# Kernel optimization log

Hardware: AMD Instinct MI355X
Metric: run time of the kernel (lower is better)

Reference implementation:

```python
import jax, jax.numpy as jnp
import numpy as np
from jax import lax

T, B, K, H, L = 256, 64, 1024, 1024, 3

def setup_inputs() -> dict:
    key = jax.random.key(0)
    ks = jax.random.split(key, 6)
    x = jax.random.normal(ks[0], (T, B, K), dtype=jnp.float32)
    h0 = jax.random.normal(ks[1], (L, B, H), dtype=jnp.float32) * 0.1
    # xavier-ish / orthogonal-ish scale for stability
    w_ih = jax.random.normal(ks[2], (L, 3 * H, K), dtype=jnp.float32) * (1.0 / np.sqrt(K))
    w_hh = jax.random.normal(ks[3], (L, 3 * H, H), dtype=jnp.float32) * (1.0 / np.sqrt(H))
    b_ih = jnp.zeros((L, 3 * H), dtype=jnp.float32)
    b_hh = jnp.zeros((L, 3 * H), dtype=jnp.float32)
    return {"x": x, "h0": h0, "w_ih": w_ih, "w_hh": w_hh, "b_ih": b_ih, "b_hh": b_hh}

def _gru_layer(x_seq, h_init, wih, whh, bih, bhh):
    # x_seq: [T,B,Kin], h_init: [B,H], wih: [3H,Kin], whh: [3H,H]
    Hd = h_init.shape[-1]
    # precompute input-to-hidden projections for all timesteps in one GEMM
    gi = jnp.einsum('tbk,gk->tbg', x_seq, wih) + bih  # [T,B,3H]

    def step(h, gi_t):
        gh = h @ whh.T + bhh  # [B,3H]
        r = jax.nn.sigmoid(gi_t[:, :Hd] + gh[:, :Hd])
        z = jax.nn.sigmoid(gi_t[:, Hd:2 * Hd] + gh[:, Hd:2 * Hd])
        n = jnp.tanh(gi_t[:, 2 * Hd:] + r * gh[:, 2 * Hd:])
        h_new = (1.0 - z) * n + z * h
        return h_new, h_new

    h_last, outs = lax.scan(step, h_init, gi)
    return h_last, outs  # [B,H], [T,B,H]

def reference(x, h0, w_ih, w_hh, b_ih, b_hh):
    layer_in = x
    h_n = []
    for l in range(w_ih.shape[0]):
        h_last, layer_in = _gru_layer(layer_in, h0[l], w_ih[l], w_hh[l], b_ih[l], b_hh[l])
        h_n.append(h_last)
    return jnp.stack(h_n, axis=0)  # [L,B,H]
```

## Files before the change

### kernel.cpp

```cpp
#include <hip/hip_runtime.h>
#include <hip/hip_bf16.h>

typedef __attribute__((ext_vector_type(8))) short bf16x8;
typedef __attribute__((ext_vector_type(4))) float f32x4;

#define T_STEPS 256
#define BATCH   64
#define KDIM    1024
#define HDIM    1024
#define NGATE   3072
#define LAYERS  3
#define SLOTE   (BATCH * HDIM)
#define RING_SLOTS (T_STEPS + 1)
#define WSZ     (192L * 32 * 64 * 8)
#define FSTRIDE 4

#define LDS_BS_BYTES  65536
#define LDS_WIS_BYTES 65536
#define LDS_GI_BYTES  (2 * 3 * 64 * 16 * 4)
#define LDS_TOTAL (LDS_BS_BYTES + LDS_WIS_BYTES + LDS_GI_BYTES)

#define MFMA16(a, b, c) __builtin_amdgcn_mfma_f32_16x16x32_bf16(a, b, c, 0, 0, 0)

__device__ __forceinline__ unsigned short f2b(float f) {
  union { float f; unsigned int u; } a; a.f = f;
  unsigned int u = a.u;
  unsigned int r = (u + 0x7FFFu + ((u >> 16) & 1u)) >> 16;
  return (unsigned short)r;
}
__device__ __forceinline__ void gload16(const void* gptr, void* ldsptr) {
  __builtin_amdgcn_global_load_lds(
      (const __attribute__((address_space(1))) unsigned int*)gptr,
      (__attribute__((address_space(3))) unsigned int*)ldsptr,
      16, 0, 0);
}

__global__ void f2b_kernel(const float* __restrict__ src,
                           unsigned short* __restrict__ dst, int n4) {
  int i = blockIdx.x * blockDim.x + threadIdx.x;
  if (i < n4) {
    float4 v = ((const float4*)src)[i];
    ushort4 o;
    o.x = f2b(v.x); o.y = f2b(v.y); o.z = f2b(v.z); o.w = f2b(v.w);
    ((ushort4*)dst)[i] = o;
  }
}

__global__ void swizzle_w(const float* __restrict__ w,
                          unsigned short* __restrict__ out) {
  long gid = (long)blockIdx.x * 256 + threadIdx.x;
  int lane = (int)(gid & 63);
  long rest = gid >> 6;
  int kc = (int)(rest & 31); rest >>= 5;
  int ntile = (int)(rest % 192); int l = (int)(rest / 192);
  int n  = ntile * 16 + (lane & 15);
  int k0 = kc * 32 + (lane >> 4) * 8;
  const float* src = w + (((long)l * NGATE + n) * KDIM + k0);
  unsigned short o[8];
#pragma unroll
  for (int j = 0; j < 8; j++) o[j] = f2b(src[j]);
  bf16x8 v = *(bf16x8*)o;
  *(bf16x8*)(out + gid * 8) = v;
}

__global__ __launch_bounds__(512, 2) void gru_fused(
    const unsigned short* __restrict__ xb,
    const unsigned short* __restrict__ wswhh,
    const unsigned short* __restrict__ wswih,
    const float* __restrict__ bih,
    const float* __restrict__ bhh,
    const float* __restrict__ h0,
    unsigned short* __restrict__ rings,
    float* __restrict__ hout,
    unsigned int* __restrict__ flags)
{
  extern __shared__ __align__(16) char smem[];
  unsigned short* Bs  = (unsigned short*)smem;
  unsigned short* Wis = (unsigned short*)(smem + LDS_BS_BYTES);
  float* gi_lds = (float*)(smem + LDS_BS_BYTES + LDS_WIS_BYTES);

  int l = blockIdx.x >> 6, g = blockIdx.x & 63;
  int tid = threadIdx.x, wave = tid >> 6, lane = tid & 63;
  int lg = lane >> 4;
  int rg = wave & 3;
  bool is_h = (wave < 4);
  int row = rg * 16 + (lane & 15);
  int cb  = g * 16 + lg * 4;

  const unsigned short* whh_l = wswhh + (size_t)l * WSZ;
  const unsigned short* wih_l = wswih + (size_t)l * WSZ;
  unsigned short* ring_l = rings + (size_t)l * RING_SLOTS * SLOTE;
  const unsigned short* prev_ring = rings + (size_t)(l - 1) * RING_SLOTS * SLOTE;
  unsigned int* fl = flags + (size_t)l * 64 * FSTRIDE;
  const unsigned int* fp = flags + (size_t)(l > 0 ? (l - 1) : 0) * 64 * FSTRIDE;

#pragma unroll
  for (int i = 0; i < 16; i++) {
    int p = wave * 16 + i;
    int gate = (p >> 5) & 1;
    int kc = p & 31;
    const unsigned short* src = (p < 64)
        ? whh_l + ((((long)gate * 64 + g) * 32 + kc) * 64 + lane) * 8
        : wih_l + ((((long)gate * 64 + g) * 32 + kc) * 64 + lane) * 8;
    unsigned short* dst = (p < 64)
        ? &Bs[(size_t)p * 512 + (size_t)lane * 8]
        : &Wis[(size_t)(p - 64) * 512 + (size_t)lane * 8];
    gload16(src, dst);
  }

  bf16x8 wn[32];
  {
    const unsigned short* base = is_h ? whh_l : wih_l;
#pragma unroll
    for (int kc = 0; kc < 32; kc++)
      wn[kc] = *(const bf16x8*)(base + ((((long)(2 * 64 + g)) * 32 + kc) * 64 + lane) * 8);
  }

  float br_[4], bz_[4], bi_n[4], bh_n[4];
  float h[4] = {0.f, 0.f, 0.f, 0.f};
  if (is_h) {
    const float* bh_l = bhh + l * NGATE;
    const float* bi_l = bih + l * NGATE;
    float4 bhr4 = *(const float4*)(bh_l + 0 * HDIM + cb);
    float4 bhz4 = *(const float4*)(bh_l + 1 * HDIM + cb);
    float4 bhn4 = *(const float4*)(bh_l + 2 * HDIM + cb);
    float4 bir4 = *(const float4*)(bi_l + 0 * HDIM + cb);
    float4 biz4 = *(const float4*)(bi_l + 1 * HDIM + cb);
    float4 bin4 = *(const float4*)(bi_l + 2 * HDIM + cb);
    br_[0] = bir4.x + bhr4.x; br_[1] = bir4.y + bhr4.y; br_[2] = bir4.z + bhr4.z; br_[3] = bir4.w + bhr4.w;
    bz_[0] = biz4.x + bhz4.x; bz_[1] = biz4.y + bhz4.y; bz_[2] = biz4.z + bhz4.z; bz_[3] = biz4.w + bhz4.w;
    bi_n[0] = bin4.x; bi_n[1] = bin4.y; bi_n[2] = bin4.z; bi_n[3] = bin4.w;
    bh_n[0] = bhn4.x; bh_n[1] = bhn4.y; bh_n[2] = bhn4.z; bh_n[3] = bhn4.w;

    float4 h4 = *(const float4*)(h0 + (size_t)l * SLOTE + (size_t)row * HDIM + cb);
    h[0] = h4.x; h[1] = h4.y; h[2] = h4.z; h[3] = h4.w;
    union { unsigned short us[4]; unsigned long long u; } pk;
#pragma unroll
    for (int r = 0; r < 4; r++) pk.us[r] = f2b(h[r]);
    unsigned short* slotT = ring_l + (size_t)T_STEPS * SLOTE;
    __hip_atomic_store((unsigned long long*)(slotT + (size_t)g * 1024 + (size_t)row * 16 + lg * 4),
                       pk.u, __ATOMIC_RELAXED, __HIP_MEMORY_SCOPE_AGENT);
  }

  f32x4 air, aiz, ain;
  auto xgemv = [&](int tt) {
    f32x4 z = {};
    air = z; aiz = z; ain = z;
    if (l == 0) {
      const unsigned short* xa_b = xb + (size_t)tt * SLOTE + (size_t)row * KDIM + lg * 8;
#pragma unroll
      for (int kb = 0; kb < 4; kb++) {
        bf16x8 xa[8];
#pragma unroll
        for (int j = 0; j < 8; j++)
          xa[j] = *(const bf16x8*)(xa_b + (size_t)(kb * 8 + j) * 32);
#pragma unroll
        for (int j = 0; j < 8; j++) {
          int kc = kb * 8 + j;
          bf16x8 wir = *(const bf16x8*)&Wis[(size_t)kc * 512 + (size_t)lane * 8];
          bf16x8 wiz = *(const bf16x8*)&Wis[(size_t)(32 + kc) * 512 + (size_t)lane * 8];
          air = MFMA16(wir, xa[j], air);
          aiz = MFMA16(wiz, xa[j], aiz);
          ain = MFMA16(wn[kc], xa[j], ain);
        }
      }
    } else {
      const unsigned short* xa_b = prev_ring + (size_t)(T_STEPS - 1 - tt) * SLOTE
                                   + (size_t)(lg >> 1) * 1024 + (size_t)row * 16 + (lg & 1) * 8;
#pragma unroll
      for (int kb = 0; kb < 4; kb++) {
        bf16x8 xa[8];
#pragma unroll
        for (int j = 0; j < 8; j++)
          xa[j] = *(const bf16x8*)(xa_b + (size_t)(kb * 8 + j) * 2048);
#pragma unroll
        for (int j = 0; j < 8; j++) {
          int kc = kb * 8 + j;
          bf16x8 wir = *(const bf16x8*)&Wis[(size_t)kc * 512 + (size_t)lane * 8];
          bf16x8 wiz = *(const bf16x8*)&Wis[(size_t)(32 + kc) * 512 + (size_t)lane * 8];
          air = MFMA16(wir, xa[j], air);
          aiz = MFMA16(wiz, xa[j], aiz);
          ain = MFMA16(wn[kc], xa[j], ain);
        }
      }
    }
    float* gp = gi_lds + (size_t)(tt & 1) * 3072 + (size_t)row * 16 + lg * 4;
    *(f32x4*)(gp + 0)    = air;
    *(f32x4*)(gp + 1024) = aiz;
    *(f32x4*)(gp + 2048) = ain;
  };

  __syncthreads();
  if (tid == 0)
    __hip_atomic_store(&fl[g * FSTRIDE], 1u, __ATOMIC_RELAXED, __HIP_MEMORY_SCOPE_AGENT);

  if (is_h) {
    while (__hip_atomic_load(&fl[lane * FSTRIDE], __ATOMIC_RELAXED,
                             __HIP_MEMORY_SCOPE_AGENT) < 1u) {}
    asm volatile("" ::: "memory");
  } else {
    if (l > 0) {
      while (__hip_atomic_load(&fp[lane * FSTRIDE], __ATOMIC_RELAXED,
                               __HIP_MEMORY_SCOPE_AGENT) < 2u) {}
      asm volatile("" ::: "memory");
    }
    xgemv(0);
  }
  __syncthreads();

#pragma unroll 1
  for (int t = 0; t < T_STEPS; t++) {
    if (is_h) {
      const unsigned short* ha_b = ring_l + (size_t)(T_STEPS - t) * SLOTE
                                   + (size_t)(lg >> 1) * 1024 + (size_t)row * 16 + (lg & 1) * 8;
      f32x4 ahr = {}, ahz = {}, ahn = {};
#pragma unroll
      for (int kb = 0; kb < 4; kb++) {
        bf16x8 hh[8];
#pragma unroll
        for (int j = 0; j < 8; j++)
          hh[j] = *(const bf16x8*)(ha_b + (size_t)(kb * 8 + j) * 2048);
#pragma unroll
        for (int j = 0; j < 8; j++) {
          int kc = kb * 8 + j;
          bf16x8 whr = *(const bf16x8*)&Bs[(size_t)kc * 512 + (size_t)lane * 8];
          bf16x8 whz = *(const bf16x8*)&Bs[(size_t)(32 + kc) * 512 + (size_t)lane * 8];
          ahr = MFMA16(whr, hh[j], ahr);
          ahz = MFMA16(whz, hh[j], ahz);
          ahn = MFMA16(wn[kc], hh[j], ahn);
        }
      }
      const float* gp = gi_lds + (size_t)(t & 1) * 3072 + (size_t)row * 16 + lg * 4;
      f32x4 xir = *(const f32x4*)(gp + 0);
      f32x4 xiz = *(const f32x4*)(gp + 1024);
      f32x4 xin = *(const f32x4*)(gp + 2048);
      unsigned short* hn = ring_l + (size_t)(T_STEPS - 1 - t) * SLOTE;
      union { unsigned short us[4]; unsigned long long u; } pk;
#pragma unroll
      for (int r = 0; r < 4; r++) {
        float xr = xir[r] + ahr[r] + br_[r];
        float xz = xiz[r] + ahz[r] + bz_[r];
        float rr = 1.0f / (1.0f + __expf(-xr));
        float zz = 1.0f / (1.0f + __expf(-xz));
        float xn = (xin[r] + bi_n[r]) + rr * (ahn[r] + bh_n[r]);
        float e2 = __expf(-2.0f * xn);
        float nn = (1.0f - e2) / (1.0f + e2);
        float hv = (1.0f - zz) * nn + zz * h[r];
        h[r] = hv;
        pk.us[r] = f2b(hv);
      }
      __hip_atomic_store((unsigned long long*)(hn + (size_t)g * 1024 + (size_t)row * 16 + lg * 4),
                         pk.u, __ATOMIC_RELAXED, __HIP_MEMORY_SCOPE_AGENT);
      if (t == T_STEPS - 1) {
        float4 o; o.x = h[0]; o.y = h[1]; o.z = h[2]; o.w = h[3];
        *(float4*)(hout + (size_t)l * SLOTE + (size_t)row * HDIM + cb) = o;
      }
    } else if (t + 1 < T_STEPS) {
      if (l > 0) {
        while (__hip_atomic_load(&fp[lane * FSTRIDE], __ATOMIC_RELAXED,
                                 __HIP_MEMORY_SCOPE_AGENT) < (unsigned)(t + 3)) {}
        asm volatile("" ::: "memory");
      }
      xgemv(t + 1);
    }

    __syncthreads();

    if (is_h) {
      if (tid == 0)
        __hip_atomic_store(&fl[g * FSTRIDE], (unsigned)(t + 2),
                           __ATOMIC_RELAXED, __HIP_MEMORY_SCOPE_AGENT);
      if (t + 1 < T_STEPS) {
        while (__hip_atomic_load(&fl[lane * FSTRIDE], __ATOMIC_RELAXED,
                                 __HIP_MEMORY_SCOPE_AGENT) < (unsigned)(t + 2)) {}
        asm volatile("" ::: "memory");
      }
    }
  }
}

extern "C" void kernel_launch(void* const* d_in, const int* in_sizes, int n_in,
                              void* d_out, int out_size, void* d_ws, size_t ws_size,
                              hipStream_t stream) {
  const float* x   = (const float*)d_in[0];
  const float* h0  = (const float*)d_in[1];
  const float* wih = (const float*)d_in[2];
  const float* whh = (const float*)d_in[3];
  const float* bih = (const float*)d_in[4];
  const float* bhh = (const float*)d_in[5];
  float* out = (float*)d_out;

  char* p = (char*)d_ws;
  unsigned short* xb    = (unsigned short*)p; p += (size_t)T_STEPS * SLOTE * 2;
  unsigned short* wswhh = (unsigned short*)p; p += (size_t)LAYERS * WSZ * 2;
  unsigned short* wswih = (unsigned short*)p; p += (size_t)LAYERS * WSZ * 2;
  unsigned short* rings = (unsigned short*)p; p += (size_t)LAYERS * RING_SLOTS * SLOTE * 2;
  unsigned int*   flags = (unsigned int*)p;   p += 4096;

  static int attr_set = 0;
  if (!attr_set) {
    hipFuncSetAttribute((const void*)gru_fused,
                        hipFuncAttributeMaxDynamicSharedMemorySize, LDS_TOTAL);
    attr_set = 1;
  }

  hipMemsetAsync(flags, 0, 4096, stream);
  f2b_kernel<<<16384, 256, 0, stream>>>(x, xb, (T_STEPS * SLOTE) / 4);
  swizzle_w<<<4608, 256, 0, stream>>>(whh, wswhh);
  swizzle_w<<<4608, 256, 0, stream>>>(wih, wswih);

  gru_fused<<<LAYERS * 64, 512, LDS_TOTAL, stream>>>(
      xb, wswhh, wswih, bih, bhh, h0, rings, out, flags);
}
```

Baseline: 2.340 ms.

## Move hidden n-gate weights to LDS, stream input z-gate weights from global

The h-waves now read the n-gate recurrent weights from LDS instead of holding them in 32 VGPR vectors. The input-side z-gate weights are streamed from global memory on every step, and the gi exchange buffer moves from LDS to a per-block global workspace. The h-path also issues all 32 hidden-state loads before its MFMA chain, to expose more memory-level parallelism on the serial critical path. The intent is to cut register pressure and shorten the recurrent step, at the cost of more global traffic in the x-waves and gi round-trips through global/L2 instead of LDS.

```diff
diff --git a/kernel.cpp b/kernel.cpp
--- a/kernel.cpp
+++ b/kernel.cpp
@@ -16,9 +16,9 @@
 #define FSTRIDE 4
 
 #define LDS_BS_BYTES  65536
-#define LDS_WIS_BYTES 65536
-#define LDS_GI_BYTES  (2 * 3 * 64 * 16 * 4)
-#define LDS_TOTAL (LDS_BS_BYTES + LDS_WIS_BYTES + LDS_GI_BYTES)
+#define LDS_WHN_BYTES 32768
+#define LDS_WIR_BYTES 32768
+#define LDS_TOTAL (LDS_BS_BYTES + LDS_WHN_BYTES + LDS_WIR_BYTES)
 
 #define MFMA16(a, b, c) __builtin_amdgcn_mfma_f32_16x16x32_bf16(a, b, c, 0, 0, 0)
 
@@ -71,13 +71,14 @@
     const float* __restrict__ bhh,
     const float* __restrict__ h0,
     unsigned short* __restrict__ rings,
+    float* __restrict__ giws,
     float* __restrict__ hout,
     unsigned int* __restrict__ flags)
 {
   extern __shared__ __align__(16) char smem[];
   unsigned short* Bs  = (unsigned short*)smem;
-  unsigned short* Wis = (unsigned short*)(smem + LDS_BS_BYTES);
-  float* gi_lds = (float*)(smem + LDS_BS_BYTES + LDS_WIS_BYTES);
+  unsigned short* Whn = (unsigned short*)(smem + LDS_BS_BYTES);
+  unsigned short* Wir = (unsigned short*)(smem + LDS_BS_BYTES + LDS_WHN_BYTES);
 
   int l = blockIdx.x >> 6, g = blockIdx.x & 63;
   int tid = threadIdx.x, wave = tid >> 6, lane = tid & 63;
@@ -93,27 +94,34 @@
   const unsigned short* prev_ring = rings + (size_t)(l - 1) * RING_SLOTS * SLOTE;
   unsigned int* fl = flags + (size_t)l * 64 * FSTRIDE;
   const unsigned int* fp = flags + (size_t)(l > 0 ? (l - 1) : 0) * 64 * FSTRIDE;
+  float* gi_ws = giws + (size_t)blockIdx.x * 2 * 3072;
 
 #pragma unroll
   for (int i = 0; i < 16; i++) {
-    int p = wave * 16 + i;
-    int gate = (p >> 5) & 1;
-    int kc = p & 31;
-    const unsigned short* src = (p < 64)
-        ? whh_l + ((((long)gate * 64 + g) * 32 + kc) * 64 + lane) * 8
-        : wih_l + ((((long)gate * 64 + g) * 32 + kc) * 64 + lane) * 8;
-    unsigned short* dst = (p < 64)
-        ? &Bs[(size_t)p * 512 + (size_t)lane * 8]
-        : &Wis[(size_t)(p - 64) * 512 + (size_t)lane * 8];
+    int p = wave + i * 8;
+    const unsigned short* src;
+    unsigned short* dst;
+    if (p < 64) {
+      int gate = p >> 5, kc = p & 31;
+      src = whh_l + ((((long)gate * 64 + g) * 32 + kc) * 64 + lane) * 8;
+      dst = &Bs[(size_t)p * 512 + (size_t)lane * 8];
+    } else if (p < 96) {
+      int kc = p - 64;
+      src = whh_l + ((((long)(2 * 64 + g)) * 32 + kc) * 64 + lane) * 8;
+      dst = &Whn[(size_t)kc * 512 + (size_t)lane * 8];
+    } else {
+      int kc = p - 96;
+      src = wih_l + ((((long)(0 * 64 + g)) * 32 + kc) * 64 + lane) * 8;
+      dst = &Wir[(size_t)kc * 512 + (size_t)lane * 8];
+    }
     gload16(src, dst);
   }
 
   bf16x8 wn[32];
-  {
-    const unsigned short* base = is_h ? whh_l : wih_l;
+  if (!is_h) {
 #pragma unroll
     for (int kc = 0; kc < 32; kc++)
-      wn[kc] = *(const bf16x8*)(base + ((((long)(2 * 64 + g)) * 32 + kc) * 64 + lane) * 8);
+      wn[kc] = *(const bf16x8*)(wih_l + ((((long)(2 * 64 + g)) * 32 + kc) * 64 + lane) * 8);
   }
 
   float br_[4], bz_[4], bi_n[4], bh_n[4];
@@ -142,49 +150,35 @@
                        pk.u, __ATOMIC_RELAXED, __HIP_MEMORY_SCOPE_AGENT);
   }
 
-  f32x4 air, aiz, ain;
   auto xgemv = [&](int tt) {
-    f32x4 z = {};
-    air = z; aiz = z; ain = z;
+    f32x4 air = {}, aiz = {}, ain = {};
+    const unsigned short* xa_b;
+    size_t stride;
     if (l == 0) {
-      const unsigned short* xa_b = xb + (size_t)tt * SLOTE + (size_t)row * KDIM + lg * 8;
-#pragma unroll
-      for (int kb = 0; kb < 4; kb++) {
-        bf16x8 xa[8];
-#pragma unroll
-        for (int j = 0; j < 8; j++)
-          xa[j] = *(const bf16x8*)(xa_b + (size_t)(kb * 8 + j) * 32);
-#pragma unroll
-        for (int j = 0; j < 8; j++) {
-          int kc = kb * 8 + j;
-          bf16x8 wir = *(const bf16x8*)&Wis[(size_t)kc * 512 + (size_t)lane * 8];
-          bf16x8 wiz = *(const bf16x8*)&Wis[(size_t)(32 + kc) * 512 + (size_t)lane * 8];
-          air = MFMA16(wir, xa[j], air);
-          aiz = MFMA16(wiz, xa[j], aiz);
-          ain = MFMA16(wn[kc], xa[j], ain);
-        }
-      }
+      xa_b = xb + (size_t)tt * SLOTE + (size_t)row * KDIM + lg * 8;
+      stride = 32;
     } else {
-      const unsigned short* xa_b = prev_ring + (size_t)(T_STEPS - 1 - tt) * SLOTE
-                                   + (size_t)(lg >> 1) * 1024 + (size_t)row * 16 + (lg & 1) * 8;
-#pragma unroll
-      for (int kb = 0; kb < 4; kb++) {
-        bf16x8 xa[8];
-#pragma unroll
-        for (int j = 0; j < 8; j++)
-          xa[j] = *(const bf16x8*)(xa_b + (size_t)(kb * 8 + j) * 2048);
-#pragma unroll
-        for (int j = 0; j < 8; j++) {
-          int kc = kb * 8 + j;
-          bf16x8 wir = *(const bf16x8*)&Wis[(size_t)kc * 512 + (size_t)lane * 8];
-          bf16x8 wiz = *(const bf16x8*)&Wis[(size_t)(32 + kc) * 512 + (size_t)lane * 8];
-          air = MFMA16(wir, xa[j], air);
-          aiz = MFMA16(wiz, xa[j], aiz);
-          ain = MFMA16(wn[kc], xa[j], ain);
-        }
-      }
-    }
-    float* gp = gi_lds + (size_t)(tt & 1) * 3072 + (size_t)row * 16 + lg * 4;
+      xa_b = prev_ring + (size_t)(T_STEPS - 1 - tt) * SLOTE
+             + (size_t)(lg >> 1) * 1024 + (size_t)row * 16 + (lg & 1) * 8;
+      stride = 2048;
+    }
+#pragma unroll
+    for (int half = 0; half < 2; half++) {
+      bf16x8 xa[16];
+#pragma unroll
+      for (int j = 0; j < 16; j++)
+        xa[j] = *(const bf16x8*)(xa_b + (size_t)(half * 16 + j) * stride);
+#pragma unroll
+      for (int j = 0; j < 16; j++) {
+        int kc = half * 16 + j;
+        bf16x8 wir = *(const bf16x8*)&Wir[(size_t)kc * 512 + (size_t)lane * 8];
+        bf16x8 wiz = *(const bf16x8*)(wih_l + ((((long)(1 * 64 + g)) * 32 + kc) * 64 + lane) * 8);
+        air = MFMA16(wir, xa[j], air);
+        aiz = MFMA16(wiz, xa[j], aiz);
+        ain = MFMA16(wn[kc], xa[j], ain);
+      }
+    }
+    float* gp = gi_ws + (size_t)(tt & 1) * 3072 + (size_t)row * 16 + lg * 4;
     *(f32x4*)(gp + 0)    = air;
     *(f32x4*)(gp + 1024) = aiz;
     *(f32x4*)(gp + 2048) = ain;
@@ -213,27 +207,27 @@
     if (is_h) {
       const unsigned short* ha_b = ring_l + (size_t)(T_STEPS - t) * SLOTE
                                    + (size_t)(lg >> 1) * 1024 + (size_t)row * 16 + (lg & 1) * 8;
-      f32x4 ahr = {}, ahz = {}, ahn = {};
-#pragma unroll
-      for (int kb = 0; kb < 4; kb++) {
-        bf16x8 hh[8];
-#pragma unroll
-        for (int j = 0; j < 8; j++)
-          hh[j] = *(const bf16x8*)(ha_b + (size_t)(kb * 8 + j) * 2048);
-#pragma unroll
-        for (int j = 0; j < 8; j++) {
-          int kc = kb * 8 + j;
-          bf16x8 whr = *(const bf16x8*)&Bs[(size_t)kc * 512 + (size_t)lane * 8];
-          bf16x8 whz = *(const bf16x8*)&Bs[(size_t)(32 + kc) * 512 + (size_t)lane * 8];
-          ahr = MFMA16(whr, hh[j], ahr);
-          ahz = MFMA16(whz, hh[j], ahz);
-          ahn = MFMA16(wn[kc], hh[j], ahn);
-        }
-      }
-      const float* gp = gi_lds + (size_t)(t & 1) * 3072 + (size_t)row * 16 + lg * 4;
+      bf16x8 ha[32];
+#pragma unroll
+      for (int kc = 0; kc < 32; kc++)
+        ha[kc] = *(const bf16x8*)(ha_b + (size_t)kc * 2048);
+
+      const float* gp = gi_ws + (size_t)(t & 1) * 3072 + (size_t)row * 16 + lg * 4;
       f32x4 xir = *(const f32x4*)(gp + 0);
       f32x4 xiz = *(const f32x4*)(gp + 1024);
       f32x4 xin = *(const f32x4*)(gp + 2048);
+
+      f32x4 ahr = {}, ahz = {}, ahn = {};
+#pragma unroll
+      for (int kc = 0; kc < 32; kc++) {
+        bf16x8 whr = *(const bf16x8*)&Bs[(size_t)kc * 512 + (size_t)lane * 8];
+        bf16x8 whz = *(const bf16x8*)&Bs[(size_t)(32 + kc) * 512 + (size_t)lane * 8];
+        bf16x8 whn = *(const bf16x8*)&Whn[(size_t)kc * 512 + (size_t)lane * 8];
+        ahr = MFMA16(whr, ha[kc], ahr);
+        ahz = MFMA16(whz, ha[kc], ahz);
+        ahn = MFMA16(whn, ha[kc], ahn);
+      }
+
       unsigned short* hn = ring_l + (size_t)(T_STEPS - 1 - t) * SLOTE;
       union { unsigned short us[4]; unsigned long long u; } pk;
 #pragma unroll
@@ -296,6 +290,7 @@
   unsigned short* wswih = (unsigned short*)p; p += (size_t)LAYERS * WSZ * 2;
   unsigned short* rings = (unsigned short*)p; p += (size_t)LAYERS * RING_SLOTS * SLOTE * 2;
   unsigned int*   flags = (unsigned int*)p;   p += 4096;
+  float*          giws  = (float*)p;          p += (size_t)192 * 2 * 3072 * 4;
 
   static int attr_set = 0;
   if (!attr_set) {
@@ -310,5 +305,5 @@
   swizzle_w<<<4608, 256, 0, stream>>>(wih, wswih);
 
   gru_fused<<<LAYERS * 64, 512, LDS_TOTAL, stream>>>(
-      xb, wswhh, wswih, bih, bhh, h0, rings, out, flags);
-}
+      xb, wswhh, wswih, bih, bhh, h0, rings, giws, out, flags);
+}
```

New measurement: 3.099 ms. 1.32x slower.

## Replace per-step workgroup barriers with LDS counter handshakes between h and x waves

Applied to the files above, without the earlier changes.

Removes the __syncthreads at each timestep and uses LDS atomic counters instead. Producer/consumer counters guard the double-buffered gi staging area, and a separate counter gathers the four h-waves before the inter-block flag is published. The h-waves can then start the next recurrent step without waiting for the x-projection waves, and those waves can run ahead by one buffer. The gi LDS rows are padded from 16 to 20 floats to reduce bank conflicts. The cost is spin-waiting on LDS atomics, plus memory-ordering subtleties in the handshake.

```diff
diff --git a/kernel.cpp b/kernel.cpp
--- a/kernel.cpp
+++ b/kernel.cpp
@@ -17,8 +17,10 @@
 
 #define LDS_BS_BYTES  65536
 #define LDS_WIS_BYTES 65536
-#define LDS_GI_BYTES  (2 * 3 * 64 * 16 * 4)
-#define LDS_TOTAL (LDS_BS_BYTES + LDS_WIS_BYTES + LDS_GI_BYTES)
+#define GI_PAR_FLOATS (3 * 64 * 20)
+#define LDS_GI_BYTES  (2 * GI_PAR_FLOATS * 4)
+#define LDS_CTRL_OFF  (LDS_BS_BYTES + LDS_WIS_BYTES + LDS_GI_BYTES)
+#define LDS_TOTAL     (LDS_CTRL_OFF + 32)
 
 #define MFMA16(a, b, c) __builtin_amdgcn_mfma_f32_16x16x32_bf16(a, b, c, 0, 0, 0)
 
@@ -78,6 +80,7 @@
   unsigned short* Bs  = (unsigned short*)smem;
   unsigned short* Wis = (unsigned short*)(smem + LDS_BS_BYTES);
   float* gi_lds = (float*)(smem + LDS_BS_BYTES + LDS_WIS_BYTES);
+  unsigned int* ctrl = (unsigned int*)(smem + LDS_CTRL_OFF);
 
   int l = blockIdx.x >> 6, g = blockIdx.x & 63;
   int tid = threadIdx.x, wave = tid >> 6, lane = tid & 63;
@@ -93,6 +96,8 @@
   const unsigned short* prev_ring = rings + (size_t)(l - 1) * RING_SLOTS * SLOTE;
   unsigned int* fl = flags + (size_t)l * 64 * FSTRIDE;
   const unsigned int* fp = flags + (size_t)(l > 0 ? (l - 1) : 0) * 64 * FSTRIDE;
+
+  if (tid < 8) ctrl[tid] = 0;
 
 #pragma unroll
   for (int i = 0; i < 16; i++) {
@@ -142,10 +147,8 @@
                        pk.u, __ATOMIC_RELAXED, __HIP_MEMORY_SCOPE_AGENT);
   }
 
-  f32x4 air, aiz, ain;
   auto xgemv = [&](int tt) {
-    f32x4 z = {};
-    air = z; aiz = z; ain = z;
+    f32x4 air = {}, aiz = {}, ain = {};
     if (l == 0) {
       const unsigned short* xa_b = xb + (size_t)tt * SLOTE + (size_t)row * KDIM + lg * 8;
 #pragma unroll
@@ -184,10 +187,16 @@
         }
       }
     }
-    float* gp = gi_lds + (size_t)(tt & 1) * 3072 + (size_t)row * 16 + lg * 4;
+    unsigned tgt = 4u * (unsigned)(tt >> 1);
+    while (__hip_atomic_load(&ctrl[3 + (tt & 1)], __ATOMIC_ACQUIRE,
+                             __HIP_MEMORY_SCOPE_WORKGROUP) < tgt) {}
+    float* gp = gi_lds + (size_t)(tt & 1) * GI_PAR_FLOATS + (size_t)row * 20 + lg * 4;
     *(f32x4*)(gp + 0)    = air;
-    *(f32x4*)(gp + 1024) = aiz;
-    *(f32x4*)(gp + 2048) = ain;
+    *(f32x4*)(gp + 1280) = aiz;
+    *(f32x4*)(gp + 2560) = ain;
+    if (lane == 0)
+      __hip_atomic_fetch_add(&ctrl[1 + (tt & 1)], 1u, __ATOMIC_RELEASE,
+                             __HIP_MEMORY_SCOPE_WORKGROUP);
   };
 
   __syncthreads();
@@ -206,11 +215,23 @@
     }
     xgemv(0);
   }
-  __syncthreads();
 
 #pragma unroll 1
   for (int t = 0; t < T_STEPS; t++) {
     if (is_h) {
+      while (__hip_atomic_load(&ctrl[1 + (t & 1)], __ATOMIC_ACQUIRE,
+                               __HIP_MEMORY_SCOPE_WORKGROUP)
+             < 4u * (unsigned)((t >> 1) + 1)) {}
+      const float* gp = gi_lds + (size_t)(t & 1) * GI_PAR_FLOATS + (size_t)row * 20 + lg * 4;
+      f32x4 xir = *(const f32x4*)(gp + 0);
+      f32x4 xiz = *(const f32x4*)(gp + 1280);
+      f32x4 xin = *(const f32x4*)(gp + 2560);
+      asm volatile("s_waitcnt lgkmcnt(0)" ::: "memory");
+      __builtin_amdgcn_sched_barrier(0);
+      if (lane == 0)
+        __hip_atomic_fetch_add(&ctrl[3 + (t & 1)], 1u, __ATOMIC_RELEASE,
+                               __HIP_MEMORY_SCOPE_WORKGROUP);
+
       const unsigned short* ha_b = ring_l + (size_t)(T_STEPS - t) * SLOTE
                                    + (size_t)(lg >> 1) * 1024 + (size_t)row * 16 + (lg & 1) * 8;
       f32x4 ahr = {}, ahz = {}, ahn = {};
@@ -230,10 +251,7 @@
           ahn = MFMA16(wn[kc], hh[j], ahn);
         }
       }
-      const float* gp = gi_lds + (size_t)(t & 1) * 3072 + (size_t)row * 16 + lg * 4;
-      f32x4 xir = *(const f32x4*)(gp + 0);
-      f32x4 xiz = *(const f32x4*)(gp + 1024);
-      f32x4 xin = *(const f32x4*)(gp + 2048);
+
       unsigned short* hn = ring_l + (size_t)(T_STEPS - 1 - t) * SLOTE;
       union { unsigned short us[4]; unsigned long long u; } pk;
 #pragma unroll
@@ -255,6 +273,25 @@
         float4 o; o.x = h[0]; o.y = h[1]; o.z = h[2]; o.w = h[3];
         *(float4*)(hout + (size_t)l * SLOTE + (size_t)row * HDIM + cb) = o;
       }
+
+      asm volatile("s_waitcnt vmcnt(0)" ::: "memory");
+      if (lane == 0)
+        __hip_atomic_fetch_add(&ctrl[0], 1u, __ATOMIC_RELEASE,
+                               __HIP_MEMORY_SCOPE_WORKGROUP);
+      if (wave == 0) {
+        while (__hip_atomic_load(&ctrl[0], __ATOMIC_ACQUIRE,
+                                 __HIP_MEMORY_SCOPE_WORKGROUP)
+               < 4u * (unsigned)(t + 1)) {}
+        asm volatile("" ::: "memory");
+        if (tid == 0)
+          __hip_atomic_store(&fl[g * FSTRIDE], (unsigned)(t + 2),
+                             __ATOMIC_RELAXED, __HIP_MEMORY_SCOPE_AGENT);
+      }
+      if (t + 1 < T_STEPS) {
+        while (__hip_atomic_load(&fl[lane * FSTRIDE], __ATOMIC_RELAXED,
+                                 __HIP_MEMORY_SCOPE_AGENT) < (unsigned)(t + 2)) {}
+        asm volatile("" ::: "memory");
+      }
     } else if (t + 1 < T_STEPS) {
       if (l > 0) {
         while (__hip_atomic_load(&fp[lane * FSTRIDE], __ATOMIC_RELAXED,
@@ -262,19 +299,6 @@
         asm volatile("" ::: "memory");
       }
       xgemv(t + 1);
-    }
-
-    __syncthreads();
-
-    if (is_h) {
-      if (tid == 0)
-        __hip_atomic_store(&fl[g * FSTRIDE], (unsigned)(t + 2),
-                           __ATOMIC_RELAXED, __HIP_MEMORY_SCOPE_AGENT);
-      if (t + 1 < T_STEPS) {
-        while (__hip_atomic_load(&fl[lane * FSTRIDE], __ATOMIC_RELAXED,
-                                 __HIP_MEMORY_SCOPE_AGENT) < (unsigned)(t + 2)) {}
-        asm volatile("" ::: "memory");
-      }
     }
   }
 }
```

Result: slower. 2.739 ms (+17.1%).
